# Optimization experiments

Measured on AMD Instinct MI355X. Metric: run time of the kernel, lower is better.

The kernel has to match this reference:

```python
import jax, jax.numpy as jnp
import numpy as np

N = 100000   # nodes
E = 3200000  # edges (avg degree 32)
D = 128      # input feature dim


def setup_inputs() -> dict:
    key = jax.random.key(0)
    ks = jax.random.split(key, 9)
    x = jax.random.normal(ks[0], (N, D), dtype=jnp.float32)
    edge_index = jax.random.randint(ks[1], (2, E), 0, N, dtype=jnp.int32)
    s = 0.05
    W1 = jax.random.normal(ks[2], (D, 64), dtype=jnp.float32) * s
    b1 = jnp.zeros((64,), dtype=jnp.float32)
    W2 = jax.random.normal(ks[3], (64, 32), dtype=jnp.float32) * s
    b2 = jnp.zeros((32,), dtype=jnp.float32)
    Wfc = jax.random.normal(ks[4], (32, 1), dtype=jnp.float32) * s
    bfc = jnp.zeros((1,), dtype=jnp.float32)
    return {"x": x, "edge_index": edge_index, "W1": W1, "b1": b1,
            "W2": W2, "b2": b2, "Wfc": Wfc, "bfc": bfc}


def _gcn_layer(x, W, b, src, dst, n):
    # GCNConv: h = D^{-1/2} (A + I) D^{-1/2} (x W) + b
    h = x @ W  # [n, out]
    loop = jnp.arange(n, dtype=src.dtype)
    src2 = jnp.concatenate([src, loop])  # add self-loops
    dst2 = jnp.concatenate([dst, loop])
    deg = jax.ops.segment_sum(jnp.ones_like(dst2, dtype=h.dtype), dst2,
                              num_segments=n)  # >= 1 due to self-loops
    dis = jax.lax.rsqrt(deg)
    norm = dis[src2] * dis[dst2]  # [E+n]
    msgs = h[src2] * norm[:, None]  # gather + scale
    return jax.ops.segment_sum(msgs, dst2, num_segments=n) + b


def reference(x, edge_index, W1, b1, W2, b2, Wfc, bfc):
    src, dst = edge_index[0], edge_index[1]
    n = x.shape[0]
    h = jax.nn.relu(_gcn_layer(x, W1, b1, src, dst, n))
    h = jax.nn.relu(_gcn_layer(h, W2, b2, src, dst, n))
    return h @ Wfc + bfc  # [n, 1]
```

## Files before the change

### kernel.cpp

```cpp
#include <hip/hip_runtime.h>
#include <hip/hip_bf16.h>
#include <hip/hip_fp16.h>


#define SCAN_CHUNK 1024
#define BSHIFT 7
#define BSIZE 128
#define B1 256
#define CSR_CAP 5120

__device__ inline void f4fma(float4& a, float s, const float4& b) {
    a.x = fmaf(s, b.x, a.x); a.y = fmaf(s, b.y, a.y);
    a.z = fmaf(s, b.z, a.z); a.w = fmaf(s, b.w, a.w);
}
__device__ inline void f4add(float4& a, const float4& b) {
    a.x += b.x; a.y += b.y; a.z += b.z; a.w += b.w;
}
__device__ inline void f4red(float4& a, int off) {
    a.x += __shfl_xor(a.x, off); a.y += __shfl_xor(a.y, off);
    a.z += __shfl_xor(a.z, off); a.w += __shfl_xor(a.w, off);
}
__device__ inline void h8load(const __half* p, float4& a, float4& b) {
    uint4 r = *(const uint4*)p;
    __half2* h = (__half2*)&r;
    float2 f0 = __half22float2(h[0]);
    float2 f1 = __half22float2(h[1]);
    float2 f2 = __half22float2(h[2]);
    float2 f3 = __half22float2(h[3]);
    a = make_float4(f0.x, f0.y, f1.x, f1.y);
    b = make_float4(f2.x, f2.y, f3.x, f3.y);
}
__device__ inline void h4store(__half* p, float4 v) {
    __half2 a = __floats2half2_rn(v.x, v.y);
    __half2 b = __floats2half2_rn(v.z, v.w);
    uint2 r; r.x = *(uint*)&a; r.y = *(uint*)&b;
    *(uint2*)p = r;
}

__global__ void k_gscan1(const int* __restrict__ in, int* __restrict__ part, int m) {
    int t = threadIdx.x;
    int base = blockIdx.x * SCAN_CHUNK + t * 4;
    int s = 0;
    for (int u = 0; u < 4; ++u) { int i = base + u; if (i < m) s += in[i]; }
    for (int o = 32; o; o >>= 1) s += __shfl_down(s, o);
    __shared__ int ws[4];
    if ((t & 63) == 0) ws[t >> 6] = s;
    __syncthreads();
    if (t == 0) part[blockIdx.x] = ws[0] + ws[1] + ws[2] + ws[3];
}

__global__ void k_gscan2(const int* __restrict__ in, const int* __restrict__ part,
                         int* __restrict__ out, int m, int nblk) {
    int t = threadIdx.x;
    int b = blockIdx.x;
    int pv = (t < b && t < nblk) ? part[t] : 0;
    int ps = pv;
    for (int o = 32; o; o >>= 1) ps += __shfl_down(ps, o);
    __shared__ int sh[4];
    if ((t & 63) == 0) sh[t >> 6] = ps;
    __syncthreads();
    int blockoff = sh[0] + sh[1] + sh[2] + sh[3];

    int base = b * SCAN_CHUNK + t * 4;
    int v0 = 0, v1 = 0, v2 = 0, v3 = 0;
    if (base + 0 < m) v0 = in[base + 0];
    if (base + 1 < m) v1 = in[base + 1];
    if (base + 2 < m) v2 = in[base + 2];
    if (base + 3 < m) v3 = in[base + 3];
    int tot = v0 + v1 + v2 + v3;
    int lane = t & 63, wid = t >> 6;
    int incl = tot;
    for (int o = 1; o < 64; o <<= 1) { int u = __shfl_up(incl, o); if (lane >= o) incl += u; }
    int excl = incl - tot;
    __shared__ int wt[4];
    if (lane == 63) wt[wid] = incl;
    __syncthreads();
    int woff = 0;
    for (int w = 0; w < wid; ++w) woff += wt[w];
    int off = blockoff + woff + excl;
    if (base + 0 < m) out[base + 0] = off;
    if (base + 1 < m) out[base + 1] = off + v0;
    if (base + 2 < m) out[base + 2] = off + v0 + v1;
    if (base + 3 < m) out[base + 3] = off + v0 + v1 + v2;
}

__global__ __launch_bounds__(256) void k_hist(const int* __restrict__ dst,
                                              int* __restrict__ ghist,
                                              int e, int echunk, int nbuck) {
    extern __shared__ int h[];
    int t = threadIdx.x, b = blockIdx.x;
    for (int i = t; i < nbuck; i += 256) h[i] = 0;
    __syncthreads();
    int s = b * echunk, epd = min(e, s + echunk);
    for (int i = s + t * 4; i < epd; i += 1024) {
        if (i + 3 < epd) {
            int4 d4 = *(const int4*)&dst[i];
            atomicAdd(&h[d4.x >> BSHIFT], 1);
            atomicAdd(&h[d4.y >> BSHIFT], 1);
            atomicAdd(&h[d4.z >> BSHIFT], 1);
            atomicAdd(&h[d4.w >> BSHIFT], 1);
        } else {
            for (int u = i; u < epd; ++u) atomicAdd(&h[dst[u] >> BSHIFT], 1);
        }
    }
    __syncthreads();
    for (int k = t; k < nbuck; k += 256)
        ghist[k * B1 + b] = h[k];
}

__global__ __launch_bounds__(256) void k_binscatter(
        const int* __restrict__ src, const int* __restrict__ dst,
        const int* __restrict__ ghist_s, int* __restrict__ ebuf,
        int e, int echunk, int nbuck) {
    extern __shared__ int cur[];
    int t = threadIdx.x, b = blockIdx.x;
    for (int k = t; k < nbuck; k += 256)
        cur[k] = ghist_s[k * B1 + b];
    __syncthreads();
    int s = b * echunk, epd = min(e, s + echunk);
    for (int i = s + t * 4; i < epd; i += 1024) {
        if (i + 3 < epd) {
            int4 d4 = *(const int4*)&dst[i];
            int4 s4 = *(const int4*)&src[i];
            int p0 = atomicAdd(&cur[d4.x >> BSHIFT], 1);
            int p1 = atomicAdd(&cur[d4.y >> BSHIFT], 1);
            int p2 = atomicAdd(&cur[d4.z >> BSHIFT], 1);
            int p3 = atomicAdd(&cur[d4.w >> BSHIFT], 1);
            ebuf[p0] = (s4.x << BSHIFT) | (d4.x & (BSIZE - 1));
            ebuf[p1] = (s4.y << BSHIFT) | (d4.y & (BSIZE - 1));
            ebuf[p2] = (s4.z << BSHIFT) | (d4.z & (BSIZE - 1));
            ebuf[p3] = (s4.w << BSHIFT) | (d4.w & (BSIZE - 1));
        } else {
            for (int u = i; u < epd; ++u) {
                int d = dst[u];
                int pos = atomicAdd(&cur[d >> BSHIFT], 1);
                ebuf[pos] = (src[u] << BSHIFT) | (d & (BSIZE - 1));
            }
        }
    }
}

__global__ __launch_bounds__(256) void k_csr(
        const int* __restrict__ ebuf, const int* __restrict__ ghist_s,
        int* __restrict__ ebuf2, int* __restrict__ rowptr, int* __restrict__ degi,
        float* __restrict__ dis, int n, int e, int nbuck) {
    int k = blockIdx.x, t = threadIdx.x;
    int estart = ghist_s[k * B1];
    int eend = (k + 1 < nbuck) ? ghist_s[(k + 1) * B1] : e;
    int ecnt = eend - estart;
    __shared__ int ein[CSR_CAP];
    __shared__ int eout[CSR_CAP];
    __shared__ int cnt[BSIZE];
    __shared__ int cur[BSIZE];
    __shared__ int wt[4];
    if (t < BSIZE) cnt[t] = 0;
    bool staged = (ecnt <= CSR_CAP);
    if (staged) {
        for (int i = t; i < ecnt; i += 256) ein[i] = ebuf[estart + i];
    }
    __syncthreads();
    if (staged) {
        for (int i = t; i < ecnt; i += 256)
            atomicAdd(&cnt[ein[i] & (BSIZE - 1)], 1);
    } else {
        for (int i = estart + t; i < eend; i += 256)
            atomicAdd(&cnt[ebuf[i] & (BSIZE - 1)], 1);
    }
    __syncthreads();
    int v = (t < BSIZE) ? cnt[t] : 0;
    int lane = t & 63, wid = t >> 6;
    int incl = v;
    for (int o = 1; o < 64; o <<= 1) { int u = __shfl_up(incl, o); if (lane >= o) incl += u; }
    if (lane == 63) wt[wid] = incl;
    __syncthreads();
    int woff = (wid == 1) ? wt[0] : 0;
    int excl = woff + incl - v;
    if (t < BSIZE) {
        cur[t] = excl;
        int node = k * BSIZE + t;
        if (node < n) {
            rowptr[node] = estart + excl;
            degi[node]   = v;
            dis[node]    = rsqrtf((float)(v + 1));
        }
    }
    __syncthreads();
    if (staged) {
        for (int i = t; i < ecnt; i += 256) {
            int w = ein[i];
            int pos = atomicAdd(&cur[w & (BSIZE - 1)], 1);
            eout[pos] = w;
        }
        __syncthreads();
        for (int i = t; i < ecnt; i += 256)
            ebuf2[estart + i] = eout[i];
    } else {
        for (int i = estart + t; i < eend; i += 256) {
            int w = ebuf[i];
            int pos = estart + atomicAdd(&cur[w & (BSIZE - 1)], 1);
            ebuf2[pos] = w;
        }
    }
}

#define SA 132
__global__ __launch_bounds__(256) void k_gemm1(
        const float* __restrict__ x, const float* __restrict__ W1,
        const float* __restrict__ dis, __half* __restrict__ h1s, int n) {
    __shared__ float Xs[64 * SA];
    __shared__ float Ws[128 * 64];
    int t = threadIdx.x;
    int nbase = blockIdx.x * 64;
    for (int i = t; i < 2048; i += 256)
        ((float4*)Ws)[i] = ((const float4*)W1)[i];
    for (int i = t; i < 2048; i += 256) {
        int row = i >> 5, q = i & 31;
        int r = nbase + row; if (r >= n) r = n - 1;
        float4 v = ((const float4*)(x + (size_t)r * 128))[q];
        *(float4*)&Xs[row * SA + q * 4] = v;
    }
    __syncthreads();
    int wid = t >> 6, lane = t & 63;
    int lx = lane & 7, ly = lane >> 3;
    int wm = wid & 1, wn = wid >> 1;
    int row0 = wm * 32 + ly * 4;
    int col0 = wn * 32 + lx * 4;
    float4 acc0 = {0.f,0.f,0.f,0.f}, acc1 = acc0, acc2 = acc0, acc3 = acc0;
#pragma unroll 4
    for (int k4 = 0; k4 < 32; ++k4) {
        int k = k4 * 4;
        float4 a0 = *(const float4*)&Xs[(row0 + 0) * SA + k];
        float4 a1 = *(const float4*)&Xs[(row0 + 1) * SA + k];
        float4 a2 = *(const float4*)&Xs[(row0 + 2) * SA + k];
        float4 a3 = *(const float4*)&Xs[(row0 + 3) * SA + k];
        float4 b0 = *(const float4*)&Ws[(k + 0) * 64 + col0];
        float4 b1 = *(const float4*)&Ws[(k + 1) * 64 + col0];
        float4 b2 = *(const float4*)&Ws[(k + 2) * 64 + col0];
        float4 b3 = *(const float4*)&Ws[(k + 3) * 64 + col0];
        f4fma(acc0, a0.x, b0); f4fma(acc0, a0.y, b1); f4fma(acc0, a0.z, b2); f4fma(acc0, a0.w, b3);
        f4fma(acc1, a1.x, b0); f4fma(acc1, a1.y, b1); f4fma(acc1, a1.z, b2); f4fma(acc1, a1.w, b3);
        f4fma(acc2, a2.x, b0); f4fma(acc2, a2.y, b1); f4fma(acc2, a2.z, b2); f4fma(acc2, a2.w, b3);
        f4fma(acc3, a3.x, b0); f4fma(acc3, a3.y, b1); f4fma(acc3, a3.z, b2); f4fma(acc3, a3.w, b3);
    }
    int grow = nbase + row0;
#pragma unroll
    for (int r = 0; r < 4; ++r) {
        int rr = grow + r;
        if (rr < n) {
            float d = dis[rr];
            float4 o = (r == 0) ? acc0 : (r == 1) ? acc1 : (r == 2) ? acc2 : acc3;
            o.x *= d; o.y *= d; o.z *= d; o.w *= d;
            h4store(&h1s[(size_t)rr * 64 + col0], o);
        }
    }
}

__global__ __launch_bounds__(256) void k_agg12(
        const __half* __restrict__ h1s, const int* __restrict__ ents,
        const int* __restrict__ rowptr, const int* __restrict__ degi,
        const float* __restrict__ dis, const float* __restrict__ b1,
        const float* __restrict__ W2, __half* __restrict__ h2s, int n) {
    __shared__ float h1row[4][72];
    int wid = threadIdx.x >> 6, lane = threadIdx.x & 63;
    int v = blockIdx.x * 4 + wid;
    int vc = min(v, n - 1);
    int start = rowptr[vc], cnt = degi[vc];
    int eg = lane >> 3;
    int fq = (lane & 7) * 8;
    int c = lane & 31, hh = lane >> 5;
    float w2r[32];
#pragma unroll
    for (int j = 0; j < 32; ++j)
        w2r[j] = W2[(hh * 32 + j) * 32 + c];
    float4 accA = {0.f, 0.f, 0.f, 0.f}, accB = accA;
    if (cnt > 0 && cnt <= 64) {
        int pre = ents[start + min(lane, cnt - 1)];
        int ng = cnt >> 3;
#pragma unroll 2
        for (int g = 0; g < ng; ++g) {
            unsigned s = ((unsigned)__shfl(pre, g * 8 + eg)) >> BSHIFT;
            float4 a, b; h8load(&h1s[(size_t)s * 64 + fq], a, b);
            f4add(accA, a); f4add(accB, b);
        }
        int rem = cnt & 7, j0 = cnt & ~7;
        if (rem) {
            unsigned s = ((unsigned)__shfl(pre, j0 + (eg < rem ? eg : 0))) >> BSHIFT;
            float4 a, b; h8load(&h1s[(size_t)s * 64 + fq], a, b);
            if (eg < rem) { f4add(accA, a); f4add(accB, b); }
        }
    } else if (cnt > 64) {
        int j = 0;
        for (; j + 8 <= cnt; j += 8) {
            unsigned s = ((unsigned)ents[start + j + eg]) >> BSHIFT;
            float4 a, b; h8load(&h1s[(size_t)s * 64 + fq], a, b);
            f4add(accA, a); f4add(accB, b);
        }
        int rem = cnt - j;
        if (rem) {
            unsigned s = ((unsigned)ents[start + j + (eg < rem ? eg : 0)]) >> BSHIFT;
            float4 a, b; h8load(&h1s[(size_t)s * 64 + fq], a, b);
            if (eg < rem) { f4add(accA, a); f4add(accB, b); }
        }
    }
    if (eg == 0) {
        float4 a, b; h8load(&h1s[(size_t)vc * 64 + fq], a, b);
        f4add(accA, a); f4add(accB, b);
    }
    f4red(accA, 8);  f4red(accB, 8);
    f4red(accA, 16); f4red(accB, 16);
    f4red(accA, 32); f4red(accB, 32);
    float d = dis[vc];
    if (eg == 0) {
        float4 bq0 = *(const float4*)&b1[fq];
        float4 bq1 = *(const float4*)&b1[fq + 4];
        float4 o0, o1;
        o0.x = fmaxf(fmaf(d, accA.x, bq0.x), 0.f);
        o0.y = fmaxf(fmaf(d, accA.y, bq0.y), 0.f);
        o0.z = fmaxf(fmaf(d, accA.z, bq0.z), 0.f);
        o0.w = fmaxf(fmaf(d, accA.w, bq0.w), 0.f);
        o1.x = fmaxf(fmaf(d, accB.x, bq1.x), 0.f);
        o1.y = fmaxf(fmaf(d, accB.y, bq1.y), 0.f);
        o1.z = fmaxf(fmaf(d, accB.z, bq1.z), 0.f);
        o1.w = fmaxf(fmaf(d, accB.w, bq1.w), 0.f);
        *(float4*)&h1row[wid][fq] = o0;
        *(float4*)&h1row[wid][fq + 4] = o1;
    }
    __syncthreads();
    float p = 0.f;
#pragma unroll
    for (int j = 0; j < 32; j += 4) {
        float4 hv = *(const float4*)&h1row[wid][hh * 32 + j];
        p = fmaf(hv.x, w2r[j + 0], p);
        p = fmaf(hv.y, w2r[j + 1], p);
        p = fmaf(hv.z, w2r[j + 2], p);
        p = fmaf(hv.w, w2r[j + 3], p);
    }
    p += __shfl_xor(p, 32);
    if (hh == 0 && v < n) h2s[(size_t)v * 32 + c] = __float2half(p * d);
}

__global__ void k_agg2(const __half* __restrict__ h2s, const int* __restrict__ ents,
                       const int* __restrict__ rowptr, const int* __restrict__ degi,
                       const float* __restrict__ dis, const float* __restrict__ b2,
                       const float* __restrict__ Wfc, const float* __restrict__ bfc,
                       float* __restrict__ out, int n) {
    int wid = threadIdx.x >> 6, lane = threadIdx.x & 63;
    int v = blockIdx.x * 4 + wid;
    if (v >= n) return;
    int start = rowptr[v], cnt = degi[v];
    int eg = lane >> 2;
    int fq = (lane & 3) * 8;
    float4 accA = {0.f, 0.f, 0.f, 0.f}, accB = accA;
    if (cnt > 0 && cnt <= 64) {
        int pre = ents[start + min(lane, cnt - 1)];
        int ng = cnt >> 4;
#pragma unroll 2
        for (int g = 0; g < ng; ++g) {
            unsigned s = ((unsigned)__shfl(pre, g * 16 + eg)) >> BSHIFT;
            float4 a, b; h8load(&h2s[(size_t)s * 32 + fq], a, b);
            f4add(accA, a); f4add(accB, b);
        }
        int rem = cnt & 15, j0 = cnt & ~15;
        if (rem) {
            unsigned s = ((unsigned)__shfl(pre, j0 + (eg < rem ? eg : 0))) >> BSHIFT;
            float4 a, b; h8load(&h2s[(size_t)s * 32 + fq], a, b);
            if (eg < rem) { f4add(accA, a); f4add(accB, b); }
        }
    } else if (cnt > 64) {
        int j = 0;
        for (; j + 16 <= cnt; j += 16) {
            unsigned s = ((unsigned)ents[start + j + eg]) >> BSHIFT;
            float4 a, b; h8load(&h2s[(size_t)s * 32 + fq], a, b);
            f4add(accA, a); f4add(accB, b);
        }
        int rem = cnt - j;
        if (rem) {
            unsigned s = ((unsigned)ents[start + j + (eg < rem ? eg : 0)]) >> BSHIFT;
            float4 a, b; h8load(&h2s[(size_t)s * 32 + fq], a, b);
            if (eg < rem) { f4add(accA, a); f4add(accB, b); }
        }
    }
    if (eg == 0) {
        float4 a, b; h8load(&h2s[(size_t)v * 32 + fq], a, b);
        f4add(accA, a); f4add(accB, b);
    }
    f4red(accA, 4);  f4red(accB, 4);
    f4red(accA, 8);  f4red(accB, 8);
    f4red(accA, 16); f4red(accB, 16);
    f4red(accA, 32); f4red(accB, 32);
    float p = 0.f;
    if (eg == 0) {
        float d = dis[v];
        float4 bq0 = *(const float4*)&b2[fq];
        float4 bq1 = *(const float4*)&b2[fq + 4];
        float4 wq0 = *(const float4*)&Wfc[fq];
        float4 wq1 = *(const float4*)&Wfc[fq + 4];
        p  = fmaxf(fmaf(d, accA.x, bq0.x), 0.f) * wq0.x;
        p += fmaxf(fmaf(d, accA.y, bq0.y), 0.f) * wq0.y;
        p += fmaxf(fmaf(d, accA.z, bq0.z), 0.f) * wq0.z;
        p += fmaxf(fmaf(d, accA.w, bq0.w), 0.f) * wq0.w;
        p += fmaxf(fmaf(d, accB.x, bq1.x), 0.f) * wq1.x;
        p += fmaxf(fmaf(d, accB.y, bq1.y), 0.f) * wq1.y;
        p += fmaxf(fmaf(d, accB.z, bq1.z), 0.f) * wq1.z;
        p += fmaxf(fmaf(d, accB.w, bq1.w), 0.f) * wq1.w;
    }
    p += __shfl_xor(p, 1); p += __shfl_xor(p, 2);
    if (lane == 0) out[v] = p + bfc[0];
}

extern "C" void kernel_launch(void* const* d_in, const int* in_sizes, int n_in,
                              void* d_out, int out_size, void* d_ws, size_t ws_size,
                              hipStream_t stream) {
    const float* x   = (const float*)d_in[0];
    const int*   ei  = (const int*)d_in[1];
    const float* W1  = (const float*)d_in[2];
    const float* b1  = (const float*)d_in[3];
    const float* W2  = (const float*)d_in[4];
    const float* b2  = (const float*)d_in[5];
    const float* Wfc = (const float*)d_in[6];
    const float* bfc = (const float*)d_in[7];
    float* out = (float*)d_out;

    const int n = in_sizes[0] / 128;
    const int e = in_sizes[1] / 2;
    const int* src = ei;
    const int* dst = ei + e;

    const int nbuck = (n + BSIZE - 1) / BSIZE;
    const int m = nbuck * B1;
    const int echunk = (e + B1 - 1) / B1;

    char* p = (char*)d_ws;
    size_t off = 0;
    auto carve = [&](size_t bytes) { void* r = p + off; off = (off + bytes + 255) & ~(size_t)255; return r; };
    int*   ghist   = (int*)  carve((size_t)m * 4);
    int*   ghist_s = (int*)  carve((size_t)m * 4);
    int*   part    = (int*)  carve(256 * 4);
    float* dis     = (float*)carve((size_t)n * 4);
    int*   rowptr  = (int*)  carve((size_t)n * 4);
    int*   degi    = (int*)  carve((size_t)n * 4);
    int*   ebuf2   = (int*)  carve((size_t)e * 4);
    __half* h2s    = (__half*)carve((size_t)n * 32 * 2);
    void*  ebuf_or_h1s = carve((size_t)e * 4);
    int*    ebuf = (int*)ebuf_or_h1s;
    __half* h1s  = (__half*)ebuf_or_h1s;
    (void)ws_size;

    const int nblk_scan = (m + SCAN_CHUNK - 1) / SCAN_CHUNK;
    const size_t lds_buck = (size_t)nbuck * 4;

    k_hist<<<B1, 256, lds_buck, stream>>>(dst, ghist, e, echunk, nbuck);
    k_gscan1<<<nblk_scan, 256, 0, stream>>>(ghist, part, m);
    k_gscan2<<<nblk_scan, 256, 0, stream>>>(ghist, part, ghist_s, m, nblk_scan);
    k_binscatter<<<B1, 256, lds_buck, stream>>>(src, dst, ghist_s, ebuf, e, echunk, nbuck);
    k_csr<<<nbuck, 256, 0, stream>>>(ebuf, ghist_s, ebuf2, rowptr, degi, dis, n, e, nbuck);
    k_gemm1<<<(n + 63) / 64, 256, 0, stream>>>(x, W1, dis, h1s, n);
    k_agg12<<<(n + 3) / 4, 256, 0, stream>>>(h1s, ebuf2, rowptr, degi, dis, b1, W2, h2s, n);
    k_agg2<<<(n + 3) / 4, 256, 0, stream>>>(h2s, ebuf2, rowptr, degi, dis, b2, Wfc, bfc, out, n);
}
```

Baseline: 306.6 us.

## Split fused layer-1 aggregation and W2 GEMM into separate kernels

The fused aggregate-then-multiply kernel is split in two. The first kernel aggregates layer-1 neighbours and writes the activated fp32 rows to a new global buffer. A separate persistent-grid kernel loads W2 into registers once per wave and applies it to many rows. This drops the per-wave 32-register W2 load, the shared-memory staging and the block barrier from the gather kernel, which should lighten register pressure and raise occupancy. In exchange it adds a 25.6 MB fp32 write and read and one more kernel launch. The gather loop unroll is also raised from 2 to 4 in both aggregation kernels.

```diff
diff --git a/kernel.cpp b/kernel.cpp
--- a/kernel.cpp
+++ b/kernel.cpp
@@ -255,28 +255,22 @@
     }
 }
 
-__global__ __launch_bounds__(256) void k_agg12(
+__global__ __launch_bounds__(256) void k_agg1(
         const __half* __restrict__ h1s, const int* __restrict__ ents,
         const int* __restrict__ rowptr, const int* __restrict__ degi,
         const float* __restrict__ dis, const float* __restrict__ b1,
-        const float* __restrict__ W2, __half* __restrict__ h2s, int n) {
-    __shared__ float h1row[4][72];
+        float* __restrict__ h1r, int n) {
     int wid = threadIdx.x >> 6, lane = threadIdx.x & 63;
     int v = blockIdx.x * 4 + wid;
-    int vc = min(v, n - 1);
-    int start = rowptr[vc], cnt = degi[vc];
+    if (v >= n) return;
+    int start = rowptr[v], cnt = degi[v];
     int eg = lane >> 3;
     int fq = (lane & 7) * 8;
-    int c = lane & 31, hh = lane >> 5;
-    float w2r[32];
-#pragma unroll
-    for (int j = 0; j < 32; ++j)
-        w2r[j] = W2[(hh * 32 + j) * 32 + c];
     float4 accA = {0.f, 0.f, 0.f, 0.f}, accB = accA;
     if (cnt > 0 && cnt <= 64) {
         int pre = ents[start + min(lane, cnt - 1)];
         int ng = cnt >> 3;
-#pragma unroll 2
+#pragma unroll 4
         for (int g = 0; g < ng; ++g) {
             unsigned s = ((unsigned)__shfl(pre, g * 8 + eg)) >> BSHIFT;
             float4 a, b; h8load(&h1s[(size_t)s * 64 + fq], a, b);
@@ -303,14 +297,14 @@
         }
     }
     if (eg == 0) {
-        float4 a, b; h8load(&h1s[(size_t)vc * 64 + fq], a, b);
+        float4 a, b; h8load(&h1s[(size_t)v * 64 + fq], a, b);
         f4add(accA, a); f4add(accB, b);
     }
     f4red(accA, 8);  f4red(accB, 8);
     f4red(accA, 16); f4red(accB, 16);
     f4red(accA, 32); f4red(accB, 32);
-    float d = dis[vc];
     if (eg == 0) {
+        float d = dis[v];
         float4 bq0 = *(const float4*)&b1[fq];
         float4 bq1 = *(const float4*)&b1[fq + 4];
         float4 o0, o1;
@@ -322,21 +316,41 @@
         o1.y = fmaxf(fmaf(d, accB.y, bq1.y), 0.f);
         o1.z = fmaxf(fmaf(d, accB.z, bq1.z), 0.f);
         o1.w = fmaxf(fmaf(d, accB.w, bq1.w), 0.f);
-        *(float4*)&h1row[wid][fq] = o0;
-        *(float4*)&h1row[wid][fq + 4] = o1;
-    }
-    __syncthreads();
-    float p = 0.f;
+        float* op = h1r + (size_t)v * 64 + fq;
+        *(float4*)op = o0;
+        *(float4*)(op + 4) = o1;
+    }
+}
+
+__global__ __launch_bounds__(256) void k_gemm2(
+        const float* __restrict__ h1r, const float* __restrict__ W2,
+        const float* __restrict__ dis, __half* __restrict__ h2s, int n) {
+    int wid = threadIdx.x >> 6, lane = threadIdx.x & 63;
+    int c = lane & 31, hh = lane >> 5;
+    float w2r[32];
 #pragma unroll
-    for (int j = 0; j < 32; j += 4) {
-        float4 hv = *(const float4*)&h1row[wid][hh * 32 + j];
-        p = fmaf(hv.x, w2r[j + 0], p);
-        p = fmaf(hv.y, w2r[j + 1], p);
-        p = fmaf(hv.z, w2r[j + 2], p);
-        p = fmaf(hv.w, w2r[j + 3], p);
-    }
-    p += __shfl_xor(p, 32);
-    if (hh == 0 && v < n) h2s[(size_t)v * 32 + c] = __float2half(p * d);
+    for (int j = 0; j < 32; ++j)
+        w2r[j] = W2[(hh * 32 + j) * 32 + c];
+    int nw = gridDim.x * 4;
+    int w0 = blockIdx.x * 4 + wid;
+#pragma unroll 1
+    for (int v = w0; v < n; v += nw) {
+        const float4* rp = (const float4*)(h1r + (size_t)v * 64 + hh * 32);
+        float p = 0.f;
+#pragma unroll
+        for (int q = 0; q < 8; ++q) {
+            float4 hv = rp[q];
+            p = fmaf(hv.x, w2r[q * 4 + 0], p);
+            p = fmaf(hv.y, w2r[q * 4 + 1], p);
+            p = fmaf(hv.z, w2r[q * 4 + 2], p);
+            p = fmaf(hv.w, w2r[q * 4 + 3], p);
+        }
+        p += __shfl_xor(p, 32);
+        if (hh == 0) {
+            float d = dis[v];
+            h2s[(size_t)v * 32 + c] = __float2half(p * d);
+        }
+    }
 }
 
 __global__ void k_agg2(const __half* __restrict__ h2s, const int* __restrict__ ents,
@@ -354,7 +368,7 @@
     if (cnt > 0 && cnt <= 64) {
         int pre = ents[start + min(lane, cnt - 1)];
         int ng = cnt >> 4;
-#pragma unroll 2
+#pragma unroll 4
         for (int g = 0; g < ng; ++g) {
             unsigned s = ((unsigned)__shfl(pre, g * 16 + eg)) >> BSHIFT;
             float4 a, b; h8load(&h2s[(size_t)s * 32 + fq], a, b);
@@ -441,6 +455,7 @@
     int*   degi    = (int*)  carve((size_t)n * 4);
     int*   ebuf2   = (int*)  carve((size_t)e * 4);
     __half* h2s    = (__half*)carve((size_t)n * 32 * 2);
+    float* h1r     = (float*)carve((size_t)n * 64 * 4);
     void*  ebuf_or_h1s = carve((size_t)e * 4);
     int*    ebuf = (int*)ebuf_or_h1s;
     __half* h1s  = (__half*)ebuf_or_h1s;
@@ -455,6 +470,7 @@
     k_binscatter<<<B1, 256, lds_buck, stream>>>(src, dst, ghist_s, ebuf, e, echunk, nbuck);
     k_csr<<<nbuck, 256, 0, stream>>>(ebuf, ghist_s, ebuf2, rowptr, degi, dis, n, e, nbuck);
     k_gemm1<<<(n + 63) / 64, 256, 0, stream>>>(x, W1, dis, h1s, n);
-    k_agg12<<<(n + 3) / 4, 256, 0, stream>>>(h1s, ebuf2, rowptr, degi, dis, b1, W2, h2s, n);
+    k_agg1<<<(n + 3) / 4, 256, 0, stream>>>(h1s, ebuf2, rowptr, degi, dis, b1, h1r, n);
+    k_gemm2<<<2048, 256, 0, stream>>>(h1r, W2, dis, h2s, n);
     k_agg2<<<(n + 3) / 4, 256, 0, stream>>>(h2s, ebuf2, rowptr, degi, dis, b2, Wfc, bfc, out, n);
 }
```

Result: slower. 325.8 us (+6.2%).
